# Kernel tuning notes

Measured on AMD Instinct MI355X. Metric: run time of the kernel, lower is better.

Reference implementation:

```python
import jax, jax.numpy as jnp
import numpy as np

# Static graph layout: B equal-sized graphs of N nodes, DEG random edges per node.
B, N, DEG = 128, 1024, 16
F_IN, H, C = 2, 64, 2
RATIO = 0.8
E = B * N * DEG
K1 = int(np.ceil(RATIO * N))      # 820
K2 = int(np.ceil(RATIO * K1))     # 656
K3 = int(np.ceil(RATIO * K2))     # 525


def setup_inputs() -> dict:
    key = jax.random.key(0)
    ks = jax.random.split(key, 24)
    x = jax.random.normal(ks[0], (B * N, F_IN), jnp.float32)
    edge_attr = jax.random.uniform(ks[1], (E,), jnp.float32)
    # per-graph random endpoints, offset so edges stay inside each graph
    local = jax.random.randint(ks[2], (2, B, N * DEG), 0, N)
    edge_index = (local + (jnp.arange(B) * N)[None, :, None]).reshape(2, E)

    def lin(k, i, o):
        return jax.random.normal(k, (i, o), jnp.float32) / np.sqrt(i)

    def bias(k, o):
        return jax.random.normal(k, (o,), jnp.float32) * 0.01

    return {
        "x": x, "edge_attr": edge_attr,
        "W1": lin(ks[3], F_IN, H), "b1": bias(ks[4], H),
        "Wp1": lin(ks[5], H, 1), "bp1": bias(ks[6], 1),
        "W2": lin(ks[7], H, H), "b2": bias(ks[8], H),
        "Wp2": lin(ks[9], H, 1), "bp2": bias(ks[10], 1),
        "W3": lin(ks[11], H, H), "b3": bias(ks[12], H),
        "Wp3": lin(ks[13], H, 1), "bp3": bias(ks[14], 1),
        "Wl1": lin(ks[15], 2 * H, H), "bl1": bias(ks[16], H),
        "Wl2": lin(ks[17], H, H // 2), "bl2": bias(ks[18], H // 2),
        "Wl3": lin(ks[19], H // 2, C), "bl3": bias(ks[20], C),
        "edge_index": edge_index,
    }


def gcn(x, src, dst, w, W, b):
    """PyG GCNConv with gcn_norm (self-loops weight 1)."""
    h = x @ W                                       # [BN, out]
    deg = jnp.zeros((x.shape[0],), x.dtype).at[dst].add(w) + 1.0
    dinv = jax.lax.rsqrt(deg)
    norm = dinv[src] * w * dinv[dst]                # [E]
    out = jnp.zeros_like(h).at[dst].add(norm[:, None] * h[src])
    out = out + (dinv * dinv)[:, None] * h          # self-loop term
    return out + b


def sagpool(x, alive, src, dst, Wp, bp, k):
    """SAGPool: unweighted GCN scoring, per-graph top-k, x <- x * tanh(score).
    Removed nodes/edges are kept as masked (alive=False) slots -> static shapes."""
    we = (alive[src] & alive[dst]).astype(x.dtype)
    score = gcn(x, src, dst, we, Wp, bp)[:, 0]      # [BN]
    s = jnp.where(alive, score, -jnp.inf).reshape(B, N)
    _, idx = jax.lax.top_k(s, k)                    # [B, k]
    alive_new = jnp.zeros((B, N), bool).at[jnp.arange(B)[:, None], idx].set(True).reshape(-1)
    xn = jnp.where(alive_new[:, None], x * jnp.tanh(score)[:, None], 0.0)
    return xn, alive_new


def readout(x, alive):
    """concat(global_max_pool, global_mean_pool) over alive nodes per graph."""
    xr = x.reshape(B, N, -1)
    m = alive.reshape(B, N, 1)
    mx = jnp.max(jnp.where(m, xr, -jnp.inf), axis=1)
    mn = jnp.sum(jnp.where(m, xr, 0.0), axis=1) / jnp.sum(m, axis=1).astype(x.dtype)
    return jnp.concatenate([mx, mn], axis=1)        # [B, 2*H]


def _forward(x, edge_attr, W1, b1, Wp1, bp1, W2, b2, Wp2, bp2, W3, b3, Wp3, bp3,
             Wl1, bl1, Wl2, bl2, Wl3, bl3, edge_index):
    src, dst = edge_index[0], edge_index[1]
    h = jax.nn.relu(gcn(x, src, dst, edge_attr, W1, b1))
    h, a1 = sagpool(h, jnp.ones((B * N,), bool), src, dst, Wp1, bp1, K1)
    x1 = readout(h, a1)

    ea1 = edge_attr * (a1[src] & a1[dst]).astype(x.dtype)
    h = jax.nn.relu(gcn(h, src, dst, ea1, W2, b2))
    h, a2 = sagpool(h, a1, src, dst, Wp2, bp2, K2)
    x2 = readout(h, a2)

    # conv3 is called WITHOUT edge_weight -> surviving edges get weight 1
    ea2 = (a2[src] & a2[dst]).astype(x.dtype)
    h = jax.nn.relu(gcn(h, src, dst, ea2, W3, b3))
    h, a3 = sagpool(h, a2, src, dst, Wp3, bp3, K3)
    x3 = readout(h, a3)

    g = x1 + x2 + x3
    g = jax.nn.relu(g @ Wl1 + bl1)                  # dropout: eval mode (identity)
    g = jax.nn.relu(g @ Wl2 + bl2)
    return jax.nn.log_softmax(g @ Wl3 + bl3, axis=-1)


def reference(x, edge_attr, W1, b1, Wp1, bp1, W2, b2, Wp2, bp2, W3, b3, Wp3, bp3,
              Wl1, bl1, Wl2, bl2, Wl3, bl3, edge_index):
    return _forward(x, edge_attr, W1, b1, Wp1, bp1, W2, b2, Wp2, bp2, W3, b3,
                    Wp3, bp3, Wl1, bl1, Wl2, bl2, Wl3, bl3, edge_index)
```

## Files before the change

### kernel.cpp

```cpp
#include <hip/hip_runtime.h>
#include <math.h>

#define NB 128
#define NN 1024
#define BNODES (NB*NN)
#define NE 2097152
#define EPG (NE/NB)
#define EPT (EPG/NN)
#define FH 64
#define KK1 820
#define KK2 656
#define KK3 525

__global__ __launch_bounds__(1024) void k_csr(const int* __restrict__ ei,
                                              const float* __restrict__ ea,
                                              int* __restrict__ rowptr,
                                              int2* __restrict__ csr_sw,
                                              float* __restrict__ dinvW,
                                              float* __restrict__ dinvU) {
  extern __shared__ int2 lcsr[];
  __shared__ int cnt[NN];
  __shared__ int cur[NN];
  __shared__ float wsum[NN];
  int b = blockIdx.x, t = threadIdx.x;
  int node = b*NN + t;
  cnt[t] = 0;
  wsum[t] = 0.f;
  __syncthreads();
  int ebase = b*EPG;
  int se[EPT]; int de[EPT]; float we[EPT];
  #pragma unroll
  for (int i = 0; i < EPT; ++i) {
    int e = ebase + i*NN + t;
    se[i] = ei[e];
    de[i] = ei[NE + e] - b*NN;
    we[i] = ea[e];
    atomicAdd(&cnt[de[i]], 1);
    atomicAdd(&wsum[de[i]], we[i]);
  }
  __syncthreads();
  int v = cnt[t];
  for (int off = 1; off < NN; off <<= 1) {
    int u = (t >= off) ? cnt[t - off] : 0;
    __syncthreads();
    cnt[t] += u;
    __syncthreads();
  }
  int excl = cnt[t] - v;
  rowptr[node] = ebase + excl;
  cur[t] = excl;
  dinvW[node] = rsqrtf(1.f + wsum[t]);
  dinvU[node] = rsqrtf(1.f + (float)v);
  if (b == NB-1 && t == NN-1) rowptr[BNODES] = NE;
  __syncthreads();
  #pragma unroll
  for (int i = 0; i < EPT; ++i) {
    int pos = atomicAdd(&cur[de[i]], 1);
    lcsr[pos] = make_int2(se[i], __float_as_int(we[i]));
  }
  __syncthreads();
  float4* dst4 = (float4*)(csr_sw + ebase);
  const float4* src4 = (const float4*)lcsr;
  #pragma unroll
  for (int i = 0; i < EPG/2/NN; ++i)
    dst4[i*NN + t] = src4[i*NN + t];
}

template<int MODE, bool L1S>
__global__ __launch_bounds__(1024, 8) void k_gath(
    const int* __restrict__ rowptr, const int2* __restrict__ csr_sw,
    const float* __restrict__ dinvW, const float* __restrict__ src,
    const float* __restrict__ Wl,
    const float* __restrict__ bias, const float* __restrict__ Wp,
    float* __restrict__ hA, float* __restrict__ qpart) {
  extern __shared__ float sHB[];
  __shared__ float sDW[NN];
  __shared__ float sWp[16];
  __shared__ float sB[16];
  __shared__ float sW1[32];
  int b = blockIdx.x >> 2, quarter = blockIdx.x & 3;
  int t = threadIdx.x, l4 = t & 3;
  int gbase = b*NN;
  sDW[t] = dinvW[gbase + t];
  if (t < 16) { sWp[t] = Wp[quarter*16 + t]; sB[t] = bias[quarter*16 + t]; }
  float4* sHB4 = (float4*)sHB;
  if (L1S) {
    if (t < 16) { sW1[t] = Wl[quarter*16 + t]; sW1[16 + t] = Wl[64 + quarter*16 + t]; }
    __syncthreads();
    #pragma unroll
    for (int i = 0; i < 16; ++i) {
      int el = i*1024 + t;
      int n = el >> 4, ff = el & 15;
      float x0 = src[(size_t)(gbase + n)*2];
      float x1 = src[(size_t)(gbase + n)*2 + 1];
      sHB[n*16 + ff] = x0*sW1[ff] + x1*sW1[16 + ff];
    }
  } else {
    const float4* hq4 = (const float4*)src + (size_t)quarter*BNODES*4 + (size_t)gbase*4;
    #pragma unroll
    for (int i = 0; i < 4; ++i) {
      int idx = i*1024 + t;
      sHB4[idx] = hq4[idx];
    }
  }
  __syncthreads();
  float4 bv = ((const float4*)sB)[l4];
  float4 wp = ((const float4*)sWp)[l4];
  #pragma unroll 1
  for (int pass = 0; pass < 4; ++pass) {
    int n = pass*256 + (t >> 2);
    int gn = gbase + n;
    float dd = sDW[n];
    float4 hv = sHB4[n*4 + l4];
    float dd2 = dd*dd;
    float4 acc;
    acc.x = fmaf(dd2, hv.x, bv.x);
    acc.y = fmaf(dd2, hv.y, bv.y);
    acc.z = fmaf(dd2, hv.z, bv.z);
    acc.w = fmaf(dd2, hv.w, bv.w);
    int r0 = rowptr[gn], r1 = rowptr[gn+1];
    for (int base = r0; base < r1; base += 4) {
      int sj = 0; float cj = 0.f;
      if (base + l4 < r1) {
        int2 p = csr_sw[base + l4];
        sj = p.x - gbase;
        float w = (MODE == 2) ? 1.f : __int_as_float(p.y);
        cj = sDW[sj] * w * dd;
      }
      #pragma unroll
      for (int j = 0; j < 4; ++j) {
        int s   = __shfl(sj, j, 4);
        float c = __shfl(cj, j, 4);
        float4 v = sHB4[s*4 + l4];
        acc.x = fmaf(c, v.x, acc.x);
        acc.y = fmaf(c, v.y, acc.y);
        acc.z = fmaf(c, v.z, acc.z);
        acc.w = fmaf(c, v.w, acc.w);
      }
    }
    acc.x = fmaxf(acc.x, 0.f); acc.y = fmaxf(acc.y, 0.f);
    acc.z = fmaxf(acc.z, 0.f); acc.w = fmaxf(acc.w, 0.f);
    ((float4*)hA)[(size_t)quarter*BNODES*4 + (size_t)gn*4 + l4] = acc;
    float dot = acc.x*wp.x + acc.y*wp.y + acc.z*wp.z + acc.w*wp.w;
    dot += __shfl_xor(dot, 2, 4);
    dot += __shfl_xor(dot, 1, 4);
    if (l4 == 0) qpart[quarter*BNODES + gn] = dot;
  }
}

__global__ void k_qfin(const float* __restrict__ dinvU, const float* __restrict__ qp,
                       float* __restrict__ q) {
  int i = blockIdx.x*256 + threadIdx.x;
  if (i < BNODES)
    q[i] = dinvU[i]*(qp[i] + qp[BNODES + i] + qp[2*BNODES + i] + qp[3*BNODES + i]);
}

__global__ void k_score(const int* __restrict__ rowptr, const int2* __restrict__ csr_sw,
                        const float* __restrict__ dinvU, const float* __restrict__ q,
                        const float* __restrict__ bp, float* __restrict__ score) {
  int t = threadIdx.x;
  int l16 = t & 15;
  int d = blockIdx.x*16 + (t >> 4);
  float du = dinvU[d];
  float sum = 0.f;
  if (du != 0.f) {
    int r0 = rowptr[d], r1 = rowptr[d+1];
    for (int base = r0; base < r1; base += 16)
      if (base + l16 < r1) sum += q[csr_sw[base + l16].x];
  }
  #pragma unroll
  for (int off = 8; off; off >>= 1) sum += __shfl_xor(sum, off, 16);
  if (l16 == 0) score[d] = bp[0] + du*(q[d] + sum);
}

__global__ void k_topk(const float* __restrict__ score,
                       const float* __restrict__ dinvU, int k,
                       float* __restrict__ tm, int* __restrict__ aliveN) {
  __shared__ float sc[NN];
  int b = blockIdx.x >> 2, p = blockIdx.x & 3;
  int t = threadIdx.x;
  int gbase = b*NN;
  #pragma unroll
  for (int i = 0; i < 4; ++i) {
    int n = i*256 + t;
    sc[n] = (dinvU[gbase + n] != 0.f) ? score[gbase + n] : -INFINITY;
  }
  __syncthreads();
  int n = p*256 + t;
  int node = gbase + n;
  float me = sc[n];
  float raw = score[node];
  int rank = 0;
  const float4* sc4 = (const float4*)sc;
  for (int j4 = 0; j4 < NN/4; ++j4) {
    float4 o = sc4[j4];
    int jb = j4*4;
    rank += (o.x > me) || (o.x == me && jb+0 < n);
    rank += (o.y > me) || (o.y == me && jb+1 < n);
    rank += (o.z > me) || (o.z == me && jb+2 < n);
    rank += (o.w > me) || (o.w == me && jb+3 < n);
  }
  int sel = (rank < k) ? 1 : 0;
  aliveN[node] = sel;
  tm[node] = sel ? tanhf(raw) : 0.f;
}

template<int MODE>
__global__ void k_degs(const int* __restrict__ rowptr, const int2* __restrict__ csr_sw,
                       const int* __restrict__ alive,
                       float* __restrict__ dinvW, float* __restrict__ dinvU) {
  int t = threadIdx.x;
  int l16 = t & 15;
  int d = blockIdx.x*16 + (t >> 4);
  int r0 = rowptr[d], r1 = rowptr[d+1];
  float sW = 0.f, sU = 0.f;
  for (int base = r0; base < r1; base += 16) {
    if (base + l16 < r1) {
      int2 p = csr_sw[base + l16];
      if (alive[p.x]) { sW += (MODE == 2) ? 1.f : __int_as_float(p.y); sU += 1.f; }
    }
  }
  #pragma unroll
  for (int off = 8; off; off >>= 1) {
    sW += __shfl_xor(sW, off, 16);
    sU += __shfl_xor(sU, off, 16);
  }
  if (l16 == 0) {
    bool dA = (alive[d] != 0);
    dinvW[d] = dA ? rsqrtf(1.f + sW) : 0.f;
    dinvU[d] = dA ? rsqrtf(1.f + sU) : 0.f;
  }
}

template<bool DOLIN>
__global__ void k_srl(const float* __restrict__ hA, const float* __restrict__ tm,
                      const int* __restrict__ aliveN, const float* __restrict__ W,
                      float* __restrict__ hB,
                      float* __restrict__ pmax, float* __restrict__ psum) {
  __shared__ float sX[64][65];
  __shared__ float sW[64*64];
  __shared__ float sTm[64];
  __shared__ int sAl[64];
  __shared__ float rm[4][FH], rs[4][FH];
  int t = threadIdx.x;
  int blk = blockIdx.x;
  int nb = blk*64;
  if (DOLIN)
    for (int i = t; i < 1024; i += 256) ((float4*)sW)[i] = ((const float4*)W)[i];
  if (t < 64) { sTm[t] = tm[nb + t]; sAl[t] = aliveN[nb + t]; }
  __syncthreads();
  #pragma unroll
  for (int q = 0; q < 4; ++q) {
    const float* hq = hA + (size_t)q*BNODES*16 + (size_t)nb*16;
    #pragma unroll
    for (int i = 0; i < 4; ++i) {
      int idx = i*256 + t;
      int n = idx >> 4, ff = idx & 15;
      sX[n][q*16 + ff] = hq[idx] * sTm[n];
    }
  }
  __syncthreads();
  {
    int f = t & 63, r = t >> 6;
    float mx = -INFINITY, sm = 0.f;
    #pragma unroll
    for (int i = 0; i < 16; ++i) {
      int n = r + i*4;
      float v = sX[n][f];
      if (sAl[n]) { mx = fmaxf(mx, v); sm += v; }
    }
    rm[r][f] = mx; rs[r][f] = sm;
  }
  __syncthreads();
  if (t < FH) {
    float m2 = fmaxf(fmaxf(rm[0][t], rm[1][t]), fmaxf(rm[2][t], rm[3][t]));
    float s2 = rs[0][t] + rs[1][t] + rs[2][t] + rs[3][t];
    pmax[blk*FH + t] = m2;
    psum[blk*FH + t] = s2;
  }
  if (DOLIN) {
    int node = t >> 2;
    int quarter = t & 3;
    int f0 = quarter * 16;
    float4 a0 = {0,0,0,0}, a1 = a0, a2 = a0, a3 = a0;
    #pragma unroll 4
    for (int k = 0; k < 64; ++k) {
      float xv = sX[node][k];
      const float4 w0 = *(const float4*)&sW[k*64 + f0];
      const float4 w1 = *(const float4*)&sW[k*64 + f0 + 4];
      const float4 w2 = *(const float4*)&sW[k*64 + f0 + 8];
      const float4 w3 = *(const float4*)&sW[k*64 + f0 + 12];
      a0.x = fmaf(xv, w0.x, a0.x); a0.y = fmaf(xv, w0.y, a0.y);
      a0.z = fmaf(xv, w0.z, a0.z); a0.w = fmaf(xv, w0.w, a0.w);
      a1.x = fmaf(xv, w1.x, a1.x); a1.y = fmaf(xv, w1.y, a1.y);
      a1.z = fmaf(xv, w1.z, a1.z); a1.w = fmaf(xv, w1.w, a1.w);
      a2.x = fmaf(xv, w2.x, a2.x); a2.y = fmaf(xv, w2.y, a2.y);
      a2.z = fmaf(xv, w2.z, a2.z); a2.w = fmaf(xv, w2.w, a2.w);
      a3.x = fmaf(xv, w3.x, a3.x); a3.y = fmaf(xv, w3.y, a3.y);
      a3.z = fmaf(xv, w3.z, a3.z); a3.w = fmaf(xv, w3.w, a3.w);
    }
    float4* dst = (float4*)(hB + (size_t)quarter*BNODES*16 + (size_t)(nb + node)*16);
    dst[0] = a0; dst[1] = a1; dst[2] = a2; dst[3] = a3;
  }
}

__global__ void k_mlp(const float* __restrict__ pmax, const float* __restrict__ psum,
                      const float* __restrict__ Wl1, const float* __restrict__ bl1,
                      const float* __restrict__ Wl2, const float* __restrict__ bl2,
                      const float* __restrict__ Wl3, const float* __restrict__ bl3,
                      float* __restrict__ out) {
  __shared__ float sg[2*FH];
  __shared__ float l1[FH];
  __shared__ float l2[FH/2];
  __shared__ float l3[2];
  int b = blockIdx.x, t = threadIdx.x;
  const float kf[3] = {(float)KK1, (float)KK2, (float)KK3};
  float gm = 0.f, gs = 0.f;
  #pragma unroll
  for (int l = 0; l < 3; ++l) {
    const float* pm = pmax + (size_t)l*NB*16*FH + (b*16)*FH;
    const float* ps = psum + (size_t)l*NB*16*FH + (b*16)*FH;
    float mm = -INFINITY, ss = 0.f;
    #pragma unroll
    for (int p = 0; p < 16; ++p) {
      mm = fmaxf(mm, pm[p*FH + t]);
      ss += ps[p*FH + t];
    }
    gm += mm;
    gs += ss / kf[l];
  }
  sg[t] = gm;
  sg[FH + t] = gs;
  __syncthreads();
  float acc = bl1[t];
  #pragma unroll
  for (int k = 0; k < 2*FH; ++k) acc = fmaf(sg[k], Wl1[k*FH + t], acc);
  l1[t] = fmaxf(acc, 0.f);
  __syncthreads();
  if (t < 32) {
    float a2 = bl2[t];
    #pragma unroll
    for (int k = 0; k < FH; ++k) a2 = fmaf(l1[k], Wl2[k*32 + t], a2);
    l2[t] = fmaxf(a2, 0.f);
  }
  __syncthreads();
  if (t < 2) {
    float a3 = bl3[t];
    #pragma unroll
    for (int k = 0; k < 32; ++k) a3 = fmaf(l2[k], Wl3[k*2 + t], a3);
    l3[t] = a3;
  }
  __syncthreads();
  if (t == 0) {
    float m = fmaxf(l3[0], l3[1]);
    float lse = m + logf(expf(l3[0]-m) + expf(l3[1]-m));
    out[b*2+0] = l3[0] - lse;
    out[b*2+1] = l3[1] - lse;
  }
}

extern "C" void kernel_launch(void* const* d_in, const int* in_sizes, int n_in,
                              void* d_out, int out_size, void* d_ws, size_t ws_size,
                              hipStream_t stream) {
  const float* x   = (const float*)d_in[0];
  const float* ea  = (const float*)d_in[1];
  const float* W1  = (const float*)d_in[2];
  const float* b1  = (const float*)d_in[3];
  const float* Wp1 = (const float*)d_in[4];
  const float* bp1 = (const float*)d_in[5];
  const float* W2  = (const float*)d_in[6];
  const float* b2  = (const float*)d_in[7];
  const float* Wp2 = (const float*)d_in[8];
  const float* bp2 = (const float*)d_in[9];
  const float* W3  = (const float*)d_in[10];
  const float* b3  = (const float*)d_in[11];
  const float* Wp3 = (const float*)d_in[12];
  const float* bp3 = (const float*)d_in[13];
  const float* Wl1 = (const float*)d_in[14];
  const float* bl1 = (const float*)d_in[15];
  const float* Wl2 = (const float*)d_in[16];
  const float* bl2 = (const float*)d_in[17];
  const float* Wl3 = (const float*)d_in[18];
  const float* bl3 = (const float*)d_in[19];
  const int*   ei  = (const int*)d_in[20];
  float* out = (float*)d_out;

  int2* csr_sw = (int2*)d_ws;
  float* hA    = (float*)(csr_sw + NE);
  float* hB    = hA + (size_t)BNODES*FH;
  float* dinvW = hB + (size_t)BNODES*FH;
  float* dinvU = dinvW + BNODES;
  float* qpart = dinvU + BNODES;
  float* q     = qpart + 4*BNODES;
  float* score = q + BNODES;
  float* tm    = score + BNODES;
  float* pmax  = tm + BNODES;
  float* psum  = pmax + 3*NB*16*FH;
  int* aliveN  = (int*)(psum + 3*NB*16*FH);
  int* rowptr  = aliveN + BNODES;

  const size_t gathLds = (size_t)NN*16*sizeof(float);
  const int gS = BNODES/64;
  const int gG = BNODES/16;
  const int gN = BNODES/256;

  k_csr<<<NB, 1024, EPG*sizeof(int2), stream>>>(ei, ea, rowptr, csr_sw, dinvW, dinvU);

  k_gath<0,true><<<NB*4, 1024, gathLds, stream>>>(rowptr, csr_sw, dinvW, x, W1, b1, Wp1, hA, qpart);
  k_qfin<<<gN, 256, 0, stream>>>(dinvU, qpart, q);
  k_score<<<gG, 256, 0, stream>>>(rowptr, csr_sw, dinvU, q, bp1, score);
  k_topk<<<NB*4, 256, 0, stream>>>(score, dinvU, KK1, tm, aliveN);
  k_srl<true><<<gS, 256, 0, stream>>>(hA, tm, aliveN, W2, hB, pmax, psum);
  k_degs<1><<<gG, 256, 0, stream>>>(rowptr, csr_sw, aliveN, dinvW, dinvU);

  k_gath<1,false><<<NB*4, 1024, gathLds, stream>>>(rowptr, csr_sw, dinvW, hB, W1, b2, Wp2, hA, qpart);
  k_qfin<<<gN, 256, 0, stream>>>(dinvU, qpart, q);
  k_score<<<gG, 256, 0, stream>>>(rowptr, csr_sw, dinvU, q, bp2, score);
  k_topk<<<NB*4, 256, 0, stream>>>(score, dinvU, KK2, tm, aliveN);
  k_srl<true><<<gS, 256, 0, stream>>>(hA, tm, aliveN, W3, hB, pmax + NB*16*FH, psum + NB*16*FH);
  k_degs<2><<<gG, 256, 0, stream>>>(rowptr, csr_sw, aliveN, dinvW, dinvU);

  k_gath<2,false><<<NB*4, 1024, gathLds, stream>>>(rowptr, csr_sw, dinvW, hB, W1, b3, Wp3, hA, qpart);
  k_qfin<<<gN, 256, 0, stream>>>(dinvU, qpart, q);
  k_score<<<gG, 256, 0, stream>>>(rowptr, csr_sw, dinvU, q, bp3, score);
  k_topk<<<NB*4, 256, 0, stream>>>(score, dinvU, KK3, tm, aliveN);
  k_srl<false><<<gS, 256, 0, stream>>>(hA, tm, aliveN, W3, hB, pmax + 2*NB*16*FH, psum + 2*NB*16*FH);

  k_mlp<<<NB, FH, 0, stream>>>(pmax, psum, Wl1, bl1, Wl2, bl2, Wl3, bl3, out);
}
```

Before: 376.5 us.

## Precompute per-edge source normalization coefficients in a separate pass before gather

Adds a k_coef kernel that, before each GCN layer, writes each edge's source index together with dinv[src]*weight into a new buffer. The gather kernel then walks the edges one at a time, reading the precomputed coefficient directly, instead of having each lane group load four edges and broadcast them with shuffles. This removes the shared-memory dinv table and the shuffle traffic from the inner loop. The block-to-(graph,quarter) mapping is also changed so the four quarter-blocks of a graph are no longer adjacent. The cost is three extra kernel launches that each read and write the 16 MB edge array, plus a serial per-edge dependent load in the gather loop.

```diff
diff --git a/kernel.cpp b/kernel.cpp
--- a/kernel.cpp
+++ b/kernel.cpp
@@ -66,22 +66,30 @@
     dst4[i*NN + t] = src4[i*NN + t];
 }
 
+template<int MODE>
+__global__ void k_coef(const int2* __restrict__ csr_sw, const float* __restrict__ dinvW,
+                       int2* __restrict__ cei) {
+  int e = blockIdx.x*256 + threadIdx.x;
+  if (e >= NE) return;
+  int2 p = csr_sw[e];
+  float w = (MODE == 2) ? 1.f : __int_as_float(p.y);
+  cei[e] = make_int2(p.x, __float_as_int(dinvW[p.x] * w));
+}
+
 template<int MODE, bool L1S>
 __global__ __launch_bounds__(1024, 8) void k_gath(
-    const int* __restrict__ rowptr, const int2* __restrict__ csr_sw,
+    const int* __restrict__ rowptr, const int2* __restrict__ cei,
     const float* __restrict__ dinvW, const float* __restrict__ src,
     const float* __restrict__ Wl,
     const float* __restrict__ bias, const float* __restrict__ Wp,
     float* __restrict__ hA, float* __restrict__ qpart) {
   extern __shared__ float sHB[];
-  __shared__ float sDW[NN];
   __shared__ float sWp[16];
   __shared__ float sB[16];
   __shared__ float sW1[32];
-  int b = blockIdx.x >> 2, quarter = blockIdx.x & 3;
+  int b = blockIdx.x & (NB-1), quarter = blockIdx.x >> 7;
   int t = threadIdx.x, l4 = t & 3;
   int gbase = b*NN;
-  sDW[t] = dinvW[gbase + t];
   if (t < 16) { sWp[t] = Wp[quarter*16 + t]; sB[t] = bias[quarter*16 + t]; }
   float4* sHB4 = (float4*)sHB;
   if (L1S) {
@@ -110,7 +118,7 @@
   for (int pass = 0; pass < 4; ++pass) {
     int n = pass*256 + (t >> 2);
     int gn = gbase + n;
-    float dd = sDW[n];
+    float dd = dinvW[gn];
     float4 hv = sHB4[n*4 + l4];
     float dd2 = dd*dd;
     float4 acc;
@@ -119,24 +127,14 @@
     acc.z = fmaf(dd2, hv.z, bv.z);
     acc.w = fmaf(dd2, hv.w, bv.w);
     int r0 = rowptr[gn], r1 = rowptr[gn+1];
-    for (int base = r0; base < r1; base += 4) {
-      int sj = 0; float cj = 0.f;
-      if (base + l4 < r1) {
-        int2 p = csr_sw[base + l4];
-        sj = p.x - gbase;
-        float w = (MODE == 2) ? 1.f : __int_as_float(p.y);
-        cj = sDW[sj] * w * dd;
-      }
-      #pragma unroll
-      for (int j = 0; j < 4; ++j) {
-        int s   = __shfl(sj, j, 4);
-        float c = __shfl(cj, j, 4);
-        float4 v = sHB4[s*4 + l4];
-        acc.x = fmaf(c, v.x, acc.x);
-        acc.y = fmaf(c, v.y, acc.y);
-        acc.z = fmaf(c, v.z, acc.z);
-        acc.w = fmaf(c, v.w, acc.w);
-      }
+    for (int e = r0; e < r1; ++e) {
+      int2 p = cei[e];
+      float c = dd * __int_as_float(p.y);
+      float4 v = sHB4[(p.x - gbase)*4 + l4];
+      acc.x = fmaf(c, v.x, acc.x);
+      acc.y = fmaf(c, v.y, acc.y);
+      acc.z = fmaf(c, v.z, acc.z);
+      acc.w = fmaf(c, v.w, acc.w);
     }
     acc.x = fmaxf(acc.x, 0.f); acc.y = fmaxf(acc.y, 0.f);
     acc.z = fmaxf(acc.z, 0.f); acc.w = fmaxf(acc.w, 0.f);
@@ -386,7 +384,8 @@
   float* out = (float*)d_out;
 
   int2* csr_sw = (int2*)d_ws;
-  float* hA    = (float*)(csr_sw + NE);
+  int2* cei    = csr_sw + NE;
+  float* hA    = (float*)(cei + NE);
   float* hB    = hA + (size_t)BNODES*FH;
   float* dinvW = hB + (size_t)BNODES*FH;
   float* dinvU = dinvW + BNODES;
@@ -403,24 +402,28 @@
   const int gS = BNODES/64;
   const int gG = BNODES/16;
   const int gN = BNODES/256;
+  const int gE = NE/256;
 
   k_csr<<<NB, 1024, EPG*sizeof(int2), stream>>>(ei, ea, rowptr, csr_sw, dinvW, dinvU);
 
-  k_gath<0,true><<<NB*4, 1024, gathLds, stream>>>(rowptr, csr_sw, dinvW, x, W1, b1, Wp1, hA, qpart);
+  k_coef<0><<<gE, 256, 0, stream>>>(csr_sw, dinvW, cei);
+  k_gath<0,true><<<NB*4, 1024, gathLds, stream>>>(rowptr, cei, dinvW, x, W1, b1, Wp1, hA, qpart);
   k_qfin<<<gN, 256, 0, stream>>>(dinvU, qpart, q);
   k_score<<<gG, 256, 0, stream>>>(rowptr, csr_sw, dinvU, q, bp1, score);
   k_topk<<<NB*4, 256, 0, stream>>>(score, dinvU, KK1, tm, aliveN);
   k_srl<true><<<gS, 256, 0, stream>>>(hA, tm, aliveN, W2, hB, pmax, psum);
   k_degs<1><<<gG, 256, 0, stream>>>(rowptr, csr_sw, aliveN, dinvW, dinvU);
 
-  k_gath<1,false><<<NB*4, 1024, gathLds, stream>>>(rowptr, csr_sw, dinvW, hB, W1, b2, Wp2, hA, qpart);
+  k_coef<1><<<gE, 256, 0, stream>>>(csr_sw, dinvW, cei);
+  k_gath<1,false><<<NB*4, 1024, gathLds, stream>>>(rowptr, cei, dinvW, hB, W1, b2, Wp2, hA, qpart);
   k_qfin<<<gN, 256, 0, stream>>>(dinvU, qpart, q);
   k_score<<<gG, 256, 0, stream>>>(rowptr, csr_sw, dinvU, q, bp2, score);
   k_topk<<<NB*4, 256, 0, stream>>>(score, dinvU, KK2, tm, aliveN);
   k_srl<true><<<gS, 256, 0, stream>>>(hA, tm, aliveN, W3, hB, pmax + NB*16*FH, psum + NB*16*FH);
   k_degs<2><<<gG, 256, 0, stream>>>(rowptr, csr_sw, aliveN, dinvW, dinvU);
 
-  k_gath<2,false><<<NB*4, 1024, gathLds, stream>>>(rowptr, csr_sw, dinvW, hB, W1, b3, Wp3, hA, qpart);
+  k_coef<2><<<gE, 256, 0, stream>>>(csr_sw, dinvW, cei);
+  k_gath<2,false><<<NB*4, 1024, gathLds, stream>>>(rowptr, cei, dinvW, hB, W1, b3, Wp3, hA, qpart);
   k_qfin<<<gN, 256, 0, stream>>>(dinvU, qpart, q);
   k_score<<<gG, 256, 0, stream>>>(rowptr, csr_sw, dinvU, q, bp3, score);
   k_topk<<<NB*4, 256, 0, stream>>>(score, dinvU, KK3, tm, aliveN);
```

Measured after the change: 392.3 us. +4.2%, slower.

## Sort nodes by in-degree per graph to balance gather loops across warps

Applied to the files above, without the earlier changes.

The CSR build now computes a per-graph counting sort of nodes by in-degree, clamped to 63, into a perm array. The gather, score and degree kernels process nodes in that order so lanes in a wavefront have similar edge counts and diverge less. The gather inner loop also switches from a 4-lane cooperative load plus shuffle to each 4-lane group walking its own edges one at a time. Block indexing is swapped so quarters of the same graph run in different waves. This adds a perm lookup and makes the output writes non-contiguous.

```diff
diff --git a/kernel.cpp b/kernel.cpp
--- a/kernel.cpp
+++ b/kernel.cpp
@@ -17,15 +17,18 @@
                                               int* __restrict__ rowptr,
                                               int2* __restrict__ csr_sw,
                                               float* __restrict__ dinvW,
-                                              float* __restrict__ dinvU) {
+                                              float* __restrict__ dinvU,
+                                              int* __restrict__ perm) {
   extern __shared__ int2 lcsr[];
   __shared__ int cnt[NN];
   __shared__ int cur[NN];
   __shared__ float wsum[NN];
+  __shared__ int hist[64];
   int b = blockIdx.x, t = threadIdx.x;
   int node = b*NN + t;
   cnt[t] = 0;
   wsum[t] = 0.f;
+  if (t < 64) hist[t] = 0;
   __syncthreads();
   int ebase = b*EPG;
   int se[EPT]; int de[EPT]; float we[EPT];
@@ -52,6 +55,16 @@
   dinvW[node] = rsqrtf(1.f + wsum[t]);
   dinvU[node] = rsqrtf(1.f + (float)v);
   if (b == NB-1 && t == NN-1) rowptr[BNODES] = NE;
+  int db = min(v, 63);
+  atomicAdd(&hist[db], 1);
+  __syncthreads();
+  if (t == 0) {
+    int run = 0;
+    for (int i = 0; i < 64; ++i) { int h = hist[i]; hist[i] = run; run += h; }
+  }
+  __syncthreads();
+  int spos = atomicAdd(&hist[db], 1);
+  perm[b*NN + spos] = t;
   __syncthreads();
   #pragma unroll
   for (int i = 0; i < EPT; ++i) {
@@ -69,6 +82,7 @@
 template<int MODE, bool L1S>
 __global__ __launch_bounds__(1024, 8) void k_gath(
     const int* __restrict__ rowptr, const int2* __restrict__ csr_sw,
+    const int* __restrict__ perm,
     const float* __restrict__ dinvW, const float* __restrict__ src,
     const float* __restrict__ Wl,
     const float* __restrict__ bias, const float* __restrict__ Wp,
@@ -78,7 +92,7 @@
   __shared__ float sWp[16];
   __shared__ float sB[16];
   __shared__ float sW1[32];
-  int b = blockIdx.x >> 2, quarter = blockIdx.x & 3;
+  int b = blockIdx.x & (NB-1), quarter = blockIdx.x >> 7;
   int t = threadIdx.x, l4 = t & 3;
   int gbase = b*NN;
   sDW[t] = dinvW[gbase + t];
@@ -108,10 +122,10 @@
   float4 wp = ((const float4*)sWp)[l4];
   #pragma unroll 1
   for (int pass = 0; pass < 4; ++pass) {
-    int n = pass*256 + (t >> 2);
-    int gn = gbase + n;
-    float dd = sDW[n];
-    float4 hv = sHB4[n*4 + l4];
+    int nl = perm[gbase + pass*256 + (t >> 2)];
+    int gn = gbase + nl;
+    float dd = sDW[nl];
+    float4 hv = sHB4[nl*4 + l4];
     float dd2 = dd*dd;
     float4 acc;
     acc.x = fmaf(dd2, hv.x, bv.x);
@@ -119,24 +133,16 @@
     acc.z = fmaf(dd2, hv.z, bv.z);
     acc.w = fmaf(dd2, hv.w, bv.w);
     int r0 = rowptr[gn], r1 = rowptr[gn+1];
-    for (int base = r0; base < r1; base += 4) {
-      int sj = 0; float cj = 0.f;
-      if (base + l4 < r1) {
-        int2 p = csr_sw[base + l4];
-        sj = p.x - gbase;
-        float w = (MODE == 2) ? 1.f : __int_as_float(p.y);
-        cj = sDW[sj] * w * dd;
-      }
-      #pragma unroll
-      for (int j = 0; j < 4; ++j) {
-        int s   = __shfl(sj, j, 4);
-        float c = __shfl(cj, j, 4);
-        float4 v = sHB4[s*4 + l4];
-        acc.x = fmaf(c, v.x, acc.x);
-        acc.y = fmaf(c, v.y, acc.y);
-        acc.z = fmaf(c, v.z, acc.z);
-        acc.w = fmaf(c, v.w, acc.w);
-      }
+    for (int e = r0; e < r1; ++e) {
+      int2 p = csr_sw[e];
+      int sl = p.x - gbase;
+      float w = (MODE == 2) ? 1.f : __int_as_float(p.y);
+      float c = dd * sDW[sl] * w;
+      float4 v = sHB4[sl*4 + l4];
+      acc.x = fmaf(c, v.x, acc.x);
+      acc.y = fmaf(c, v.y, acc.y);
+      acc.z = fmaf(c, v.z, acc.z);
+      acc.w = fmaf(c, v.w, acc.w);
     }
     acc.x = fmaxf(acc.x, 0.f); acc.y = fmaxf(acc.y, 0.f);
     acc.z = fmaxf(acc.z, 0.f); acc.w = fmaxf(acc.w, 0.f);
@@ -156,11 +162,14 @@
 }
 
 __global__ void k_score(const int* __restrict__ rowptr, const int2* __restrict__ csr_sw,
+                        const int* __restrict__ perm,
                         const float* __restrict__ dinvU, const float* __restrict__ q,
                         const float* __restrict__ bp, float* __restrict__ score) {
   int t = threadIdx.x;
   int l16 = t & 15;
-  int d = blockIdx.x*16 + (t >> 4);
+  int pos = blockIdx.x*16 + (t >> 4);
+  int gb = pos & ~(NN-1);
+  int d = gb + perm[pos];
   float du = dinvU[d];
   float sum = 0.f;
   if (du != 0.f) {
@@ -207,11 +216,13 @@
 
 template<int MODE>
 __global__ void k_degs(const int* __restrict__ rowptr, const int2* __restrict__ csr_sw,
-                       const int* __restrict__ alive,
+                       const int* __restrict__ perm, const int* __restrict__ alive,
                        float* __restrict__ dinvW, float* __restrict__ dinvU) {
   int t = threadIdx.x;
   int l16 = t & 15;
-  int d = blockIdx.x*16 + (t >> 4);
+  int pos = blockIdx.x*16 + (t >> 4);
+  int gb = pos & ~(NN-1);
+  int d = gb + perm[pos];
   int r0 = rowptr[d], r1 = rowptr[d+1];
   float sW = 0.f, sU = 0.f;
   for (int base = r0; base < r1; base += 16) {
@@ -398,31 +409,32 @@
   float* psum  = pmax + 3*NB*16*FH;
   int* aliveN  = (int*)(psum + 3*NB*16*FH);
   int* rowptr  = aliveN + BNODES;
+  int* perm    = rowptr + BNODES + 2;
 
   const size_t gathLds = (size_t)NN*16*sizeof(float);
   const int gS = BNODES/64;
   const int gG = BNODES/16;
   const int gN = BNODES/256;
 
-  k_csr<<<NB, 1024, EPG*sizeof(int2), stream>>>(ei, ea, rowptr, csr_sw, dinvW, dinvU);
-
-  k_gath<0,true><<<NB*4, 1024, gathLds, stream>>>(rowptr, csr_sw, dinvW, x, W1, b1, Wp1, hA, qpart);
+  k_csr<<<NB, 1024, EPG*sizeof(int2), stream>>>(ei, ea, rowptr, csr_sw, dinvW, dinvU, perm);
+
+  k_gath<0,true><<<NB*4, 1024, gathLds, stream>>>(rowptr, csr_sw, perm, dinvW, x, W1, b1, Wp1, hA, qpart);
   k_qfin<<<gN, 256, 0, stream>>>(dinvU, qpart, q);
-  k_score<<<gG, 256, 0, stream>>>(rowptr, csr_sw, dinvU, q, bp1, score);
+  k_score<<<gG, 256, 0, stream>>>(rowptr, csr_sw, perm, dinvU, q, bp1, score);
   k_topk<<<NB*4, 256, 0, stream>>>(score, dinvU, KK1, tm, aliveN);
   k_srl<true><<<gS, 256, 0, stream>>>(hA, tm, aliveN, W2, hB, pmax, psum);
-  k_degs<1><<<gG, 256, 0, stream>>>(rowptr, csr_sw, aliveN, dinvW, dinvU);
-
-  k_gath<1,false><<<NB*4, 1024, gathLds, stream>>>(rowptr, csr_sw, dinvW, hB, W1, b2, Wp2, hA, qpart);
+  k_degs<1><<<gG, 256, 0, stream>>>(rowptr, csr_sw, perm, aliveN, dinvW, dinvU);
+
+  k_gath<1,false><<<NB*4, 1024, gathLds, stream>>>(rowptr, csr_sw, perm, dinvW, hB, W1, b2, Wp2, hA, qpart);
   k_qfin<<<gN, 256, 0, stream>>>(dinvU, qpart, q);
-  k_score<<<gG, 256, 0, stream>>>(rowptr, csr_sw, dinvU, q, bp2, score);
+  k_score<<<gG, 256, 0, stream>>>(rowptr, csr_sw, perm, dinvU, q, bp2, score);
   k_topk<<<NB*4, 256, 0, stream>>>(score, dinvU, KK2, tm, aliveN);
   k_srl<true><<<gS, 256, 0, stream>>>(hA, tm, aliveN, W3, hB, pmax + NB*16*FH, psum + NB*16*FH);
-  k_degs<2><<<gG, 256, 0, stream>>>(rowptr, csr_sw, aliveN, dinvW, dinvU);
-
-  k_gath<2,false><<<NB*4, 1024, gathLds, stream>>>(rowptr, csr_sw, dinvW, hB, W1, b3, Wp3, hA, qpart);
+  k_degs<2><<<gG, 256, 0, stream>>>(rowptr, csr_sw, perm, aliveN, dinvW, dinvU);
+
+  k_gath<2,false><<<NB*4, 1024, gathLds, stream>>>(rowptr, csr_sw, perm, dinvW, hB, W1, b3, Wp3, hA, qpart);
   k_qfin<<<gN, 256, 0, stream>>>(dinvU, qpart, q);
-  k_score<<<gG, 256, 0, stream>>>(rowptr, csr_sw, dinvU, q, bp3, score);
+  k_score<<<gG, 256, 0, stream>>>(rowptr, csr_sw, perm, dinvU, q, bp3, score);
   k_topk<<<NB*4, 256, 0, stream>>>(score, dinvU, KK3, tm, aliveN);
   k_srl<false><<<gS, 256, 0, stream>>>(hA, tm, aliveN, W3, hB, pmax + 2*NB*16*FH, psum + 2*NB*16*FH);
 
```

Result: slower. 388.2 us (+3.1%).

## Fuse degree recompute into srl kernel and simplify gather edge loop

Applied to the files above, without the earlier changes.

Removes the separate k_degs launch and folds the masked degree and dinv computation into k_srl, since both cover the same 64-node slice. The gather kernel now walks edges one at a time per 4-lane group, reading each CSR entry directly (a broadcast load) instead of loading four entries and spreading them with shuffles. Block-to-graph mapping is also changed so consecutive blocks cover different graphs of the same feature quarter. This saves launch overhead and shuffle work, at the cost of more redundant CSR loads and extra serial work inside k_srl.

```diff
diff --git a/kernel.cpp b/kernel.cpp
--- a/kernel.cpp
+++ b/kernel.cpp
@@ -78,7 +78,7 @@
   __shared__ float sWp[16];
   __shared__ float sB[16];
   __shared__ float sW1[32];
-  int b = blockIdx.x >> 2, quarter = blockIdx.x & 3;
+  int b = blockIdx.x & (NB-1), quarter = blockIdx.x >> 7;
   int t = threadIdx.x, l4 = t & 3;
   int gbase = b*NN;
   sDW[t] = dinvW[gbase + t];
@@ -119,24 +119,16 @@
     acc.z = fmaf(dd2, hv.z, bv.z);
     acc.w = fmaf(dd2, hv.w, bv.w);
     int r0 = rowptr[gn], r1 = rowptr[gn+1];
-    for (int base = r0; base < r1; base += 4) {
-      int sj = 0; float cj = 0.f;
-      if (base + l4 < r1) {
-        int2 p = csr_sw[base + l4];
-        sj = p.x - gbase;
-        float w = (MODE == 2) ? 1.f : __int_as_float(p.y);
-        cj = sDW[sj] * w * dd;
-      }
-      #pragma unroll
-      for (int j = 0; j < 4; ++j) {
-        int s   = __shfl(sj, j, 4);
-        float c = __shfl(cj, j, 4);
-        float4 v = sHB4[s*4 + l4];
-        acc.x = fmaf(c, v.x, acc.x);
-        acc.y = fmaf(c, v.y, acc.y);
-        acc.z = fmaf(c, v.z, acc.z);
-        acc.w = fmaf(c, v.w, acc.w);
-      }
+    for (int e = r0; e < r1; ++e) {
+      int2 p = csr_sw[e];
+      int sl = p.x - gbase;
+      float w = (MODE == 2) ? 1.f : __int_as_float(p.y);
+      float c = dd * sDW[sl] * w;
+      float4 v = sHB4[sl*4 + l4];
+      acc.x = fmaf(c, v.x, acc.x);
+      acc.y = fmaf(c, v.y, acc.y);
+      acc.z = fmaf(c, v.z, acc.z);
+      acc.w = fmaf(c, v.w, acc.w);
     }
     acc.x = fmaxf(acc.x, 0.f); acc.y = fmaxf(acc.y, 0.f);
     acc.z = fmaxf(acc.z, 0.f); acc.w = fmaxf(acc.w, 0.f);
@@ -205,38 +197,13 @@
   tm[node] = sel ? tanhf(raw) : 0.f;
 }
 
-template<int MODE>
-__global__ void k_degs(const int* __restrict__ rowptr, const int2* __restrict__ csr_sw,
-                       const int* __restrict__ alive,
-                       float* __restrict__ dinvW, float* __restrict__ dinvU) {
-  int t = threadIdx.x;
-  int l16 = t & 15;
-  int d = blockIdx.x*16 + (t >> 4);
-  int r0 = rowptr[d], r1 = rowptr[d+1];
-  float sW = 0.f, sU = 0.f;
-  for (int base = r0; base < r1; base += 16) {
-    if (base + l16 < r1) {
-      int2 p = csr_sw[base + l16];
-      if (alive[p.x]) { sW += (MODE == 2) ? 1.f : __int_as_float(p.y); sU += 1.f; }
-    }
-  }
-  #pragma unroll
-  for (int off = 8; off; off >>= 1) {
-    sW += __shfl_xor(sW, off, 16);
-    sU += __shfl_xor(sU, off, 16);
-  }
-  if (l16 == 0) {
-    bool dA = (alive[d] != 0);
-    dinvW[d] = dA ? rsqrtf(1.f + sW) : 0.f;
-    dinvU[d] = dA ? rsqrtf(1.f + sU) : 0.f;
-  }
-}
-
-template<bool DOLIN>
+template<bool DOLIN, int DEGMODE>
 __global__ void k_srl(const float* __restrict__ hA, const float* __restrict__ tm,
                       const int* __restrict__ aliveN, const float* __restrict__ W,
                       float* __restrict__ hB,
-                      float* __restrict__ pmax, float* __restrict__ psum) {
+                      float* __restrict__ pmax, float* __restrict__ psum,
+                      const int* __restrict__ rowptr, const int2* __restrict__ csr_sw,
+                      float* __restrict__ dinvW, float* __restrict__ dinvU) {
   __shared__ float sX[64][65];
   __shared__ float sW[64*64];
   __shared__ float sTm[64];
@@ -277,6 +244,31 @@
     float s2 = rs[0][t] + rs[1][t] + rs[2][t] + rs[3][t];
     pmax[blk*FH + t] = m2;
     psum[blk*FH + t] = s2;
+  }
+  if (DEGMODE != 0) {
+    int g = t >> 4, l16 = t & 15;
+    for (int i = 0; i < 4; ++i) {
+      int n = g*4 + i;
+      int d = nb + n;
+      int r0 = rowptr[d], r1 = rowptr[d+1];
+      float sWd = 0.f, sU = 0.f;
+      for (int base = r0; base < r1; base += 16) {
+        if (base + l16 < r1) {
+          int2 p = csr_sw[base + l16];
+          if (aliveN[p.x]) { sWd += (DEGMODE == 2) ? 1.f : __int_as_float(p.y); sU += 1.f; }
+        }
+      }
+      #pragma unroll
+      for (int off = 8; off; off >>= 1) {
+        sWd += __shfl_xor(sWd, off, 16);
+        sU  += __shfl_xor(sU, off, 16);
+      }
+      if (l16 == 0) {
+        bool dA = (sAl[n] != 0);
+        dinvW[d] = dA ? rsqrtf(1.f + sWd) : 0.f;
+        dinvU[d] = dA ? rsqrtf(1.f + sU) : 0.f;
+      }
+    }
   }
   if (DOLIN) {
     int node = t >> 2;
@@ -410,21 +402,22 @@
   k_qfin<<<gN, 256, 0, stream>>>(dinvU, qpart, q);
   k_score<<<gG, 256, 0, stream>>>(rowptr, csr_sw, dinvU, q, bp1, score);
   k_topk<<<NB*4, 256, 0, stream>>>(score, dinvU, KK1, tm, aliveN);
-  k_srl<true><<<gS, 256, 0, stream>>>(hA, tm, aliveN, W2, hB, pmax, psum);
-  k_degs<1><<<gG, 256, 0, stream>>>(rowptr, csr_sw, aliveN, dinvW, dinvU);
+  k_srl<true,1><<<gS, 256, 0, stream>>>(hA, tm, aliveN, W2, hB, pmax, psum,
+                                        rowptr, csr_sw, dinvW, dinvU);
 
   k_gath<1,false><<<NB*4, 1024, gathLds, stream>>>(rowptr, csr_sw, dinvW, hB, W1, b2, Wp2, hA, qpart);
   k_qfin<<<gN, 256, 0, stream>>>(dinvU, qpart, q);
   k_score<<<gG, 256, 0, stream>>>(rowptr, csr_sw, dinvU, q, bp2, score);
   k_topk<<<NB*4, 256, 0, stream>>>(score, dinvU, KK2, tm, aliveN);
-  k_srl<true><<<gS, 256, 0, stream>>>(hA, tm, aliveN, W3, hB, pmax + NB*16*FH, psum + NB*16*FH);
-  k_degs<2><<<gG, 256, 0, stream>>>(rowptr, csr_sw, aliveN, dinvW, dinvU);
+  k_srl<true,2><<<gS, 256, 0, stream>>>(hA, tm, aliveN, W3, hB, pmax + NB*16*FH, psum + NB*16*FH,
+                                        rowptr, csr_sw, dinvW, dinvU);
 
   k_gath<2,false><<<NB*4, 1024, gathLds, stream>>>(rowptr, csr_sw, dinvW, hB, W1, b3, Wp3, hA, qpart);
   k_qfin<<<gN, 256, 0, stream>>>(dinvU, qpart, q);
   k_score<<<gG, 256, 0, stream>>>(rowptr, csr_sw, dinvU, q, bp3, score);
   k_topk<<<NB*4, 256, 0, stream>>>(score, dinvU, KK3, tm, aliveN);
-  k_srl<false><<<gS, 256, 0, stream>>>(hA, tm, aliveN, W3, hB, pmax + 2*NB*16*FH, psum + 2*NB*16*FH);
+  k_srl<false,0><<<gS, 256, 0, stream>>>(hA, tm, aliveN, W3, hB, pmax + 2*NB*16*FH, psum + 2*NB*16*FH,
+                                         rowptr, csr_sw, dinvW, dinvU);
 
   k_mlp<<<NB, FH, 0, stream>>>(pmax, psum, Wl1, bl1, Wl2, bl2, Wl3, bl3, out);
 }
```

Measured after the change: 367.2 us. 1.03x faster.
